# Kernel optimization log

Measured on AMD Instinct MI355X. Metric: run time of the kernel, lower is better.

## Reference

```python
import jax, jax.numpy as jnp
import numpy as np

N = 100000
E = 1600000
F_IN, HID, N_CLS = 128, 16, 32


def setup_inputs() -> dict:
    key = jax.random.key(0)
    ks = jax.random.split(key, 10)
    x = jax.random.normal(ks[0], (N, F_IN), dtype=jnp.float32)
    edge_index = jax.random.randint(ks[1], (2, E), 0, N, dtype=jnp.int64)
    edge_weight = jax.random.uniform(ks[2], (E,), dtype=jnp.float32)
    def glorot(k, shape):
        lim = np.sqrt(6.0 / (shape[0] + shape[1])).astype(np.float32)
        return jax.random.uniform(k, shape, dtype=jnp.float32, minval=-lim, maxval=lim)
    return {
        'x': x, 'edge_index': edge_index, 'edge_weight': edge_weight,
        'W1_0': glorot(ks[3], (F_IN, HID)), 'W1_1': glorot(ks[4], (F_IN, HID)),
        'b1': jnp.zeros((HID,), jnp.float32),
        'W2_0': glorot(ks[5], (HID, N_CLS)), 'W2_1': glorot(ks[6], (HID, N_CLS)),
        'b2': jnp.zeros((N_CLS,), jnp.float32),
    }


def _cheb_conv_k2(x, row, col, edge_weight, W0, W1, b):
    # PyG ChebConv, K=2, lambda_max=2.0:
    #   T0 = x; T1 = L_hat x = D^{-1/2} A D^{-1/2} x - x
    n = x.shape[0]
    deg = jax.ops.segment_sum(edge_weight, row, num_segments=n)  # [N]
    dinv = jnp.where(deg > 0, jax.lax.rsqrt(deg), 0.0)
    norm = dinv[row] * edge_weight * dinv[col]                   # [E]
    agg = jax.ops.segment_sum(norm[:, None] * x[col], row, num_segments=n)  # [N,F]
    tx1 = agg - x
    return x @ W0 + tx1 @ W1 + b


def reference(x, edge_index, edge_weight, W1_0, W1_1, b1, W2_0, W2_1, b2):
    row, col = edge_index[0], edge_index[1]
    h = jax.nn.relu(_cheb_conv_k2(x, row, col, edge_weight, W1_0, W1_1, b1))
    # dropout(p=0) and DFA layers are identity in forward
    out = _cheb_conv_k2(h, row, col, edge_weight, W2_0, W2_1, b2)
    return jax.nn.log_softmax(out, axis=1)
```

## Files before the change

kernel.cpp:

```cpp
#include <hip/hip_runtime.h>
#include <hip/hip_bf16.h>


#include <hip/hip_fp16.h>

constexpr int NN   = 100000;
constexpr int NE   = 1600000;
constexpr int FIN  = 128;
constexpr int HID  = 16;
constexpr int NCLS = 32;

constexpr int RB    = 256;
constexpr int NBKT  = (NN + RB - 1) / RB;
constexpr int EPB   = 4096;
constexpr int EPT   = EPB / 256;
constexpr int GP    = (NE + EPB - 1) / EPB;
constexpr int CAP   = 8192;
constexpr int NTILE = NN / 16;

typedef float f32x2 __attribute__((ext_vector_type(2)));
typedef float f32x4 __attribute__((ext_vector_type(4)));
typedef short bf16x8 __attribute__((ext_vector_type(8)));

#if defined(__has_builtin)
#if __has_builtin(__builtin_amdgcn_cvt_pk_f32_fp8)
#define HAVE_CVT_FP8 1
#endif
#endif

static __device__ __forceinline__ unsigned int f2e4m3(float f) {
    union { float f; unsigned int u; } v; v.f = f;
    unsigned int s = (v.u >> 24) & 0x80u;
    unsigned int au = v.u & 0x7fffffffu;
    if (au > 0x43E00000u) au = 0x43E00000u;
    au += 0x7ffffu + ((au >> 20) & 1u);
    int e4 = (int)(au >> 23) - 120;
    unsigned int m = (au >> 20) & 7u;
    unsigned int byte = (e4 <= 0) ? 0u : (((unsigned int)e4 << 3) | m);
    return s | byte;
}
static __device__ __forceinline__ void fp8x4_fma(unsigned int v, float w, float* acc) {
#ifdef HAVE_CVT_FP8
    f32x2 lo = __builtin_amdgcn_cvt_pk_f32_fp8((int)v, false);
    f32x2 hi = __builtin_amdgcn_cvt_pk_f32_fp8((int)v, true);
    acc[0] += w * lo.x; acc[1] += w * lo.y;
    acc[2] += w * hi.x; acc[3] += w * hi.y;
#else
#pragma unroll
    for (int i = 0; i < 4; i++) {
        unsigned int b = (v >> (8 * i)) & 0xffu;
        float f = __int_as_float((int)(((b & 0x80u) << 24) | ((b & 0x7fu) << 20))) * 0x1p120f;
        acc[i] += w * f;
    }
#endif
}
static __device__ __forceinline__ unsigned short f2bf(float f) {
    union { float f; unsigned int u; } v; v.f = f;
    unsigned int r = v.u + 0x7fffu + ((v.u >> 16) & 1u);
    return (unsigned short)(r >> 16);
}
static __device__ __forceinline__ unsigned int wpack(float wf) {
    unsigned int b = __float_as_uint(wf) + 0x8000u;
    return (b >> 16) & 0x7fffu;
}
static __device__ __forceinline__ float wdec(unsigned int u) {
    return __uint_as_float((u >> 17) << 16);
}

__global__ void k_zero_cur(int* __restrict__ bucketCursor) {
    int i = blockIdx.x * blockDim.x + threadIdx.x;
    if (i < NBKT) bucketCursor[i] = 0;
}

__global__ __launch_bounds__(256) void k_partition(
    const int* __restrict__ row, const int* __restrict__ col,
    const float* __restrict__ w, int* __restrict__ bucketCursor,
    int2* __restrict__ partS) {
    __shared__ int2 stage[EPB];
    __shared__ unsigned short sbkt[EPB];
    __shared__ int cnt[NBKT];
    __shared__ int lofs[NBKT];
    __shared__ int cursor[NBKT];
    __shared__ int gbase[NBKT];
    __shared__ int sa[512], sb[512];
    int tid = threadIdx.x;
    long ebase = (long)blockIdx.x * EPB;
    int rr[EPT]; int cc[EPT]; float wv[EPT];
#pragma unroll
    for (int i = 0; i < EPT; i++) {
        long e = ebase + i * 256 + tid;
        if (e < NE) { rr[i] = row[e]; cc[i] = col[e]; wv[i] = w[e]; }
        else rr[i] = -1;
    }
    for (int i = tid; i < NBKT; i += 256) cnt[i] = 0;
    __syncthreads();
#pragma unroll
    for (int i = 0; i < EPT; i++)
        if (rr[i] >= 0) atomicAdd(&cnt[rr[i] >> 8], 1);
    __syncthreads();
    for (int i = tid; i < 512; i += 256) sa[i] = (i < NBKT) ? cnt[i] : 0;
    __syncthreads();
    int* src = sa; int* dst = sb;
    for (int off = 1; off < 512; off <<= 1) {
        for (int i = tid; i < 512; i += 256)
            dst[i] = src[i] + ((i >= off) ? src[i - off] : 0);
        __syncthreads();
        int* t = src; src = dst; dst = t;
    }
    for (int i = tid; i < NBKT; i += 256) {
        int ex = src[i] - cnt[i];
        lofs[i] = ex;
        cursor[i] = ex;
        int go = (cnt[i] > 0) ? atomicAdd(&bucketCursor[i], cnt[i]) : 0;
        gbase[i] = i * CAP + go;
    }
    __syncthreads();
#pragma unroll
    for (int i = 0; i < EPT; i++) {
        if (rr[i] >= 0) {
            int b = rr[i] >> 8;
            int p = atomicAdd(&cursor[b], 1);
            int2 v;
            v.x = cc[i] | ((rr[i] & 255) << 17);
            v.y = __float_as_int(wv[i]);
            stage[p] = v;
            sbkt[p] = (unsigned short)b;
        }
    }
    __syncthreads();
    int total = (int)min((long)EPB, NE - ebase);
    for (int i = tid; i < total; i += 256) {
        int b = sbkt[i];
        partS[gbase[b] + (i - lofs[b])] = stage[i];
    }
}

__global__ void k_scan_buckets(const int* __restrict__ bucketCursor,
                               int* __restrict__ bucketStart) {
    int lane = threadIdx.x;
    int v[8], e[8];
    int s = 0;
#pragma unroll
    for (int t = 0; t < 8; t++) {
        int idx = lane * 8 + t;
        v[t] = (idx < NBKT) ? bucketCursor[idx] : 0;
        e[t] = s;
        s += v[t];
    }
    int sc = s;
    for (int off = 1; off < 64; off <<= 1) {
        int up = __shfl_up(sc, off, 64);
        if (lane >= off) sc += up;
    }
    int excl = sc - s;
#pragma unroll
    for (int t = 0; t < 8; t++) {
        int idx = lane * 8 + t;
        if (idx < NBKT) bucketStart[idx] = excl + e[t];
    }
}

__global__ __launch_bounds__(256) void k_bucket_sort(
    const int2* __restrict__ partS, const int* __restrict__ bucketCursor,
    const int* __restrict__ bucketStart,
    unsigned int* __restrict__ partC, int* __restrict__ rowptr,
    float* __restrict__ dinv) {
    __shared__ int2 stage[CAP];
    __shared__ int hist[RB];
    __shared__ int cursor[RB];
    __shared__ int wtot[4];
    int b = blockIdx.x;
    int tid = threadIdx.x;
    int start = bucketStart[b];
    int count = bucketCursor[b];
    const int2* src = partS + (long)b * CAP;
    hist[tid] = 0;
    __syncthreads();
    for (int i = tid; i < count; i += 256)
        atomicAdd(&hist[(src[i].x >> 17) & 255], 1);
    __syncthreads();
    int lane = tid & 63, wv = tid >> 6;
    int v = hist[tid];
    int sc = v;
#pragma unroll
    for (int off = 1; off < 64; off <<= 1) {
        int up = __shfl_up(sc, off, 64);
        if (lane >= off) sc += up;
    }
    if (lane == 63) wtot[wv] = sc;
    __syncthreads();
    int add = 0;
    for (int w2 = 0; w2 < wv; w2++) add += wtot[w2];
    int ex = sc + add - v;
    int node = b * RB + tid;
    if (node <= NN) rowptr[node] = start + ex;
    cursor[tid] = ex;
    __syncthreads();
    for (int i = tid; i < count; i += 256) {
        int2 p = src[i];
        int rl = (p.x >> 17) & 255;
        int pos = atomicAdd(&cursor[rl], 1);
        int2 c; c.x = p.x & 0x1FFFF; c.y = p.y;
        if (pos < CAP) stage[pos] = c;
    }
    __syncthreads();
    {
        int rend = cursor[tid];
        float d = 0.f;
        for (int i = ex; i < rend; i++) d += __int_as_float(stage[i].y);
        if (node < NN) dinv[node] = d > 0.f ? rsqrtf(d) : 0.f;
    }
    for (int i = tid; i < count; i += 256)
        if (i < CAP) {
            int2 p = stage[i];
            partC[start + i] = (unsigned int)p.x | (wpack(__int_as_float(p.y)) << 17);
        }
}

__global__ __launch_bounds__(256) void k_proj1(
    const float* __restrict__ x, const float* __restrict__ W0,
    const float* __restrict__ W1, const float* __restrict__ b1,
    const float* __restrict__ dinv,
    float* __restrict__ xa, unsigned char* __restrict__ xb8) {
    int wid = (int)(((long)blockIdx.x * 256 + threadIdx.x) >> 6);
    if (wid >= NTILE) return;
    int lane = threadIdx.x & 63;
    int col = lane & 15, quad = lane >> 4;

    bf16x8 bfrag[2][4];
#pragma unroll
    for (int mat = 0; mat < 2; mat++) {
        const float* W = mat ? W1 : W0;
#pragma unroll
        for (int kb = 0; kb < 4; kb++) {
            bf16x8 f;
#pragma unroll
            for (int j = 0; j < 8; j++)
                f[j] = (short)f2bf(W[(kb * 32 + quad * 8 + j) * HID + col]);
            bfrag[mat][kb] = f;
        }
    }

    const float* xrow = x + ((long)wid * 16 + col) * FIN + quad * 8;
    float4 xb[8];
#pragma unroll
    for (int kb = 0; kb < 4; kb++) {
        xb[2 * kb]     = *(const float4*)(xrow + kb * 32);
        xb[2 * kb + 1] = *(const float4*)(xrow + kb * 32 + 4);
    }
    f32x4 acc0 = {0.f, 0.f, 0.f, 0.f}, acc1 = {0.f, 0.f, 0.f, 0.f};
#pragma unroll
    for (int kb = 0; kb < 4; kb++) {
        float4 a0 = xb[2 * kb], a1 = xb[2 * kb + 1];
        bf16x8 af;
        af[0] = (short)f2bf(a0.x); af[1] = (short)f2bf(a0.y);
        af[2] = (short)f2bf(a0.z); af[3] = (short)f2bf(a0.w);
        af[4] = (short)f2bf(a1.x); af[5] = (short)f2bf(a1.y);
        af[6] = (short)f2bf(a1.z); af[7] = (short)f2bf(a1.w);
        acc0 = __builtin_amdgcn_mfma_f32_16x16x32_bf16(af, bfrag[0][kb], acc0, 0, 0, 0);
        acc1 = __builtin_amdgcn_mfma_f32_16x16x32_bf16(af, bfrag[1][kb], acc1, 0, 0, 0);
    }

    float b1v = b1[col];
#pragma unroll
    for (int r = 0; r < 4; r++) {
        long node = (long)wid * 16 + quad * 4 + r;
        float a0 = acc0[r], a1 = acc1[r];
        xa[node * HID + col] = a0 - a1 + b1v;
        float dn = dinv[node];
        xb8[node * HID + col] = (unsigned char)f2e4m3(dn * a1);
    }
}

__global__ __launch_bounds__(256) void k_gather1(
    const int* __restrict__ rowptr, const unsigned int* __restrict__ partC,
    const float* __restrict__ dinv, const unsigned char* __restrict__ xb8,
    float* __restrict__ agg1) {
    long t = (long)blockIdx.x * 256 + threadIdx.x;
    int n = (int)(t >> 6);
    if (n >= NN) return;
    int lane = threadIdx.x & 63;
    int d = lane & 3, p = lane >> 2;
    int s = rowptr[n], e = rowptr[n + 1];
    float acc[4] = {0.f, 0.f, 0.f, 0.f};
    for (int j = s + p; j < e; j += 16) {
        unsigned int u = partC[j];
        unsigned int v = *(const unsigned int*)(xb8 + (u & 0x1FFFF) * HID + d * 4);
        fp8x4_fma(v, wdec(u), acc);
    }
#pragma unroll
    for (int i = 0; i < 4; i++) {
        acc[i] += __shfl_xor(acc[i], 4);
        acc[i] += __shfl_xor(acc[i], 8);
        acc[i] += __shfl_xor(acc[i], 16);
        acc[i] += __shfl_xor(acc[i], 32);
    }
    if (p == 0) {
        float dn = dinv[n];
        float4 o; o.x = dn * acc[0]; o.y = dn * acc[1];
        o.z = dn * acc[2]; o.w = dn * acc[3];
        *(float4*)(agg1 + (long)n * HID + d * 4) = o;
    }
}

__global__ __launch_bounds__(256) void k_proj2(
    const float* __restrict__ xa, const float* __restrict__ agg1,
    const float* __restrict__ W0, const float* __restrict__ W1,
    const float* __restrict__ b2, const float* __restrict__ dinv,
    float* __restrict__ ha, unsigned char* __restrict__ hb8) {
    long n = (long)blockIdx.x * 256 + threadIdx.x;
    if (n >= NN) return;
    float h[HID];
    const float4* xap = (const float4*)(xa + n * HID);
    const float4* agp = (const float4*)(agg1 + n * HID);
#pragma unroll
    for (int q = 0; q < 4; q++) {
        float4 a = xap[q], g = agp[q];
        h[4*q+0] = fmaxf(a.x + g.x, 0.f);
        h[4*q+1] = fmaxf(a.y + g.y, 0.f);
        h[4*q+2] = fmaxf(a.z + g.z, 0.f);
        h[4*q+3] = fmaxf(a.w + g.w, 0.f);
    }
    float accA[NCLS], accB[NCLS];
#pragma unroll
    for (int o = 0; o < NCLS; o++) { accA[o] = 0.f; accB[o] = 0.f; }
#pragma unroll 2
    for (int k = 0; k < HID; k++) {
        float hk = h[k];
#pragma unroll
        for (int o = 0; o < NCLS; o++) accA[o] += hk * W0[k * NCLS + o];
#pragma unroll
        for (int o = 0; o < NCLS; o++) accB[o] += hk * W1[k * NCLS + o];
    }
    float4* hap = (float4*)(ha + n * NCLS);
#pragma unroll
    for (int q = 0; q < 8; q++) {
        float4 va;
        va.x = accA[4*q+0] - accB[4*q+0] + b2[4*q+0];
        va.y = accA[4*q+1] - accB[4*q+1] + b2[4*q+1];
        va.z = accA[4*q+2] - accB[4*q+2] + b2[4*q+2];
        va.w = accA[4*q+3] - accB[4*q+3] + b2[4*q+3];
        hap[q] = va;
    }
    float dn = dinv[n];
    unsigned int pk[8];
#pragma unroll
    for (int q = 0; q < 8; q++)
        pk[q] = f2e4m3(dn * accB[4*q+0]) | (f2e4m3(dn * accB[4*q+1]) << 8)
              | (f2e4m3(dn * accB[4*q+2]) << 16) | (f2e4m3(dn * accB[4*q+3]) << 24);
    uint4* hbp = (uint4*)(hb8 + n * NCLS);
    hbp[0] = make_uint4(pk[0], pk[1], pk[2], pk[3]);
    hbp[1] = make_uint4(pk[4], pk[5], pk[6], pk[7]);
}

__global__ __launch_bounds__(256) void k_gather2_lsm(
    const int* __restrict__ rowptr, const unsigned int* __restrict__ partC,
    const float* __restrict__ dinv, const float* __restrict__ ha,
    const unsigned char* __restrict__ hb8, float* __restrict__ out) {
    long t = (long)blockIdx.x * 256 + threadIdx.x;
    int n = (int)(t >> 6);
    if (n >= NN) return;
    int lane = threadIdx.x & 63;
    int d = lane & 7, p = lane >> 3;
    int s = rowptr[n], e = rowptr[n + 1];
    float acc[4] = {0.f, 0.f, 0.f, 0.f};
    int j = s + p;
    for (; j + 8 < e; j += 16) {
        unsigned int u0 = partC[j], u1 = partC[j + 8];
        unsigned int v0 = *(const unsigned int*)(hb8 + (u0 & 0x1FFFF) * NCLS + d * 4);
        unsigned int v1 = *(const unsigned int*)(hb8 + (u1 & 0x1FFFF) * NCLS + d * 4);
        fp8x4_fma(v0, wdec(u0), acc);
        fp8x4_fma(v1, wdec(u1), acc);
    }
    if (j < e) {
        unsigned int u0 = partC[j];
        unsigned int v0 = *(const unsigned int*)(hb8 + (u0 & 0x1FFFF) * NCLS + d * 4);
        fp8x4_fma(v0, wdec(u0), acc);
    }
#pragma unroll
    for (int i = 0; i < 4; i++) {
        acc[i] += __shfl_xor(acc[i], 8);
        acc[i] += __shfl_xor(acc[i], 16);
        acc[i] += __shfl_xor(acc[i], 32);
    }
    float dn = dinv[n];
    float4 hv = *(const float4*)(ha + (long)n * NCLS + d * 4);
    float v0 = dn * acc[0] + hv.x;
    float v1 = dn * acc[1] + hv.y;
    float v2 = dn * acc[2] + hv.z;
    float v3 = dn * acc[3] + hv.w;
    float m = fmaxf(fmaxf(v0, v1), fmaxf(v2, v3));
    m = fmaxf(m, __shfl_xor(m, 1));
    m = fmaxf(m, __shfl_xor(m, 2));
    m = fmaxf(m, __shfl_xor(m, 4));
    float sum = __expf(v0 - m) + __expf(v1 - m) + __expf(v2 - m) + __expf(v3 - m);
    sum += __shfl_xor(sum, 1);
    sum += __shfl_xor(sum, 2);
    sum += __shfl_xor(sum, 4);
    float ls = logf(sum);
    if (p == 0) {
        float4 o; o.x = v0 - m - ls; o.y = v1 - m - ls;
        o.z = v2 - m - ls; o.w = v3 - m - ls;
        *(float4*)(out + (long)n * NCLS + d * 4) = o;
    }
}

extern "C" void kernel_launch(void* const* d_in, const int* in_sizes, int n_in,
                              void* d_out, int out_size, void* d_ws, size_t ws_size,
                              hipStream_t stream) {
    const float* x    = (const float*)d_in[0];
    const int*   ei   = (const int*)d_in[1];
    const float* ew   = (const float*)d_in[2];
    const float* W1_0 = (const float*)d_in[3];
    const float* W1_1 = (const float*)d_in[4];
    const float* b1   = (const float*)d_in[5];
    const float* W2_0 = (const float*)d_in[6];
    const float* W2_1 = (const float*)d_in[7];
    const float* b2   = (const float*)d_in[8];
    float* out = (float*)d_out;

    const int* row = ei;
    const int* col = ei + NE;

    char* ws = (char*)d_ws;
    int2*  partS     = (int2*)ws;                 ws += sizeof(int2) * (long)NBKT * CAP;
    unsigned int* partC = (unsigned int*)ws;      ws += sizeof(int) * NE;
    int*   bucketCursor = (int*)ws;               ws += sizeof(int) * NBKT;
    int*   bucketStart  = (int*)ws;               ws += sizeof(int) * NBKT;
    int*   rowptr    = (int*)ws;                  ws += sizeof(int) * (NN + 4);
    float* dinv      = (float*)ws;                ws += sizeof(float) * NN;
    float* xa        = (float*)ws;                ws += sizeof(float) * NN * HID;
    float* agg1      = (float*)ws;                ws += sizeof(float) * NN * HID;
    float* ha        = (float*)ws;                ws += sizeof(float) * NN * NCLS;
    unsigned char* xb8 = (unsigned char*)ws;      ws += sizeof(char) * NN * HID;
    unsigned char* hb8 = (unsigned char*)ws;      ws += sizeof(char) * NN * NCLS;

    k_zero_cur<<<(NBKT + 255) / 256, 256, 0, stream>>>(bucketCursor);
    k_partition<<<GP, 256, 0, stream>>>(row, col, ew, bucketCursor, partS);
    k_scan_buckets<<<1, 64, 0, stream>>>(bucketCursor, bucketStart);
    k_bucket_sort<<<NBKT, 256, 0, stream>>>(partS, bucketCursor, bucketStart,
                                            partC, rowptr, dinv);
    k_proj1<<<(NTILE * 64 + 255) / 256, 256, 0, stream>>>(x, W1_0, W1_1, b1, dinv, xa, xb8);
    {
        long th = (long)NN * 64;
        k_gather1<<<(int)((th + 255) / 256), 256, 0, stream>>>(rowptr, partC, dinv, xb8, agg1);
    }
    k_proj2<<<(NN + 255) / 256, 256, 0, stream>>>(xa, agg1, W2_0, W2_1, b2, dinv, ha, hb8);
    {
        long th = (long)NN * 64;
        k_gather2_lsm<<<(int)((th + 255) / 256), 256, 0, stream>>>(rowptr, partC, dinv, ha, hb8, out);
    }
}
```

Baseline: 232.1 us.

## Fuse gather1 with proj2, fold bucket scan into sort, drop LDS staging

Three changes. The layer-2 projection is fused into the first gather kernel: each wavefront shuffles the 16 hidden values across lanes and computes 32 outputs per weight matrix, which removes the agg1 round trip through memory and one launch. The separate single-block bucket scan kernel is removed, and each sort block instead sums the counts of all earlier buckets itself, which is redundant O(NBKT) work per block. The sort now writes partC directly from the per-row atomic positions and accumulates degree with LDS float atomics instead of staging in 64KB of shared memory. That should raise occupancy but makes the global writes scattered and the edge order within a row nondeterministic.

```diff
diff --git a/kernel.cpp b/kernel.cpp
--- a/kernel.cpp
+++ b/kernel.cpp
@@ -135,51 +135,32 @@
     }
 }
 
-__global__ void k_scan_buckets(const int* __restrict__ bucketCursor,
-                               int* __restrict__ bucketStart) {
-    int lane = threadIdx.x;
-    int v[8], e[8];
-    int s = 0;
-#pragma unroll
-    for (int t = 0; t < 8; t++) {
-        int idx = lane * 8 + t;
-        v[t] = (idx < NBKT) ? bucketCursor[idx] : 0;
-        e[t] = s;
-        s += v[t];
-    }
-    int sc = s;
-    for (int off = 1; off < 64; off <<= 1) {
-        int up = __shfl_up(sc, off, 64);
-        if (lane >= off) sc += up;
-    }
-    int excl = sc - s;
-#pragma unroll
-    for (int t = 0; t < 8; t++) {
-        int idx = lane * 8 + t;
-        if (idx < NBKT) bucketStart[idx] = excl + e[t];
-    }
-}
-
 __global__ __launch_bounds__(256) void k_bucket_sort(
     const int2* __restrict__ partS, const int* __restrict__ bucketCursor,
-    const int* __restrict__ bucketStart,
     unsigned int* __restrict__ partC, int* __restrict__ rowptr,
     float* __restrict__ dinv) {
-    __shared__ int2 stage[CAP];
     __shared__ int hist[RB];
     __shared__ int cursor[RB];
+    __shared__ float dsum[RB];
     __shared__ int wtot[4];
+    __shared__ int red[4];
     int b = blockIdx.x;
     int tid = threadIdx.x;
-    int start = bucketStart[b];
+    int lane = tid & 63, wv = tid >> 6;
+    int partial = 0;
+    for (int i = tid; i < b; i += 256) partial += bucketCursor[i];
+#pragma unroll
+    for (int off = 1; off < 64; off <<= 1) partial += __shfl_xor(partial, off, 64);
+    if (lane == 0) red[wv] = partial;
+    hist[tid] = 0;
+    dsum[tid] = 0.f;
+    __syncthreads();
+    int start = red[0] + red[1] + red[2] + red[3];
     int count = bucketCursor[b];
     const int2* src = partS + (long)b * CAP;
-    hist[tid] = 0;
-    __syncthreads();
     for (int i = tid; i < count; i += 256)
-        atomicAdd(&hist[(src[i].x >> 17) & 255], 1);
-    __syncthreads();
-    int lane = tid & 63, wv = tid >> 6;
+        atomicAdd(&hist[((unsigned)src[i].x >> 17) & 255], 1);
+    __syncthreads();
     int v = hist[tid];
     int sc = v;
 #pragma unroll
@@ -198,23 +179,17 @@
     __syncthreads();
     for (int i = tid; i < count; i += 256) {
         int2 p = src[i];
-        int rl = (p.x >> 17) & 255;
+        int rl = ((unsigned)p.x >> 17) & 255;
         int pos = atomicAdd(&cursor[rl], 1);
-        int2 c; c.x = p.x & 0x1FFFF; c.y = p.y;
-        if (pos < CAP) stage[pos] = c;
-    }
-    __syncthreads();
-    {
-        int rend = cursor[tid];
-        float d = 0.f;
-        for (int i = ex; i < rend; i++) d += __int_as_float(stage[i].y);
-        if (node < NN) dinv[node] = d > 0.f ? rsqrtf(d) : 0.f;
-    }
-    for (int i = tid; i < count; i += 256)
-        if (i < CAP) {
-            int2 p = stage[i];
-            partC[start + i] = (unsigned int)p.x | (wpack(__int_as_float(p.y)) << 17);
-        }
+        float wf = __int_as_float(p.y);
+        partC[start + pos] = ((unsigned)p.x & 0x1FFFFu) | (wpack(wf) << 17);
+        atomicAdd(&dsum[rl], wf);
+    }
+    __syncthreads();
+    if (node < NN) {
+        float dsv = dsum[tid];
+        dinv[node] = dsv > 0.f ? rsqrtf(dsv) : 0.f;
+    }
 }
 
 __global__ __launch_bounds__(256) void k_proj1(
@@ -272,10 +247,12 @@
     }
 }
 
-__global__ __launch_bounds__(256) void k_gather1(
+__global__ __launch_bounds__(256) void k_gather1_proj2(
     const int* __restrict__ rowptr, const unsigned int* __restrict__ partC,
     const float* __restrict__ dinv, const unsigned char* __restrict__ xb8,
-    float* __restrict__ agg1) {
+    const float* __restrict__ xa, const float* __restrict__ W0,
+    const float* __restrict__ W1, const float* __restrict__ b2,
+    float* __restrict__ ha, unsigned char* __restrict__ hb8) {
     long t = (long)blockIdx.x * 256 + threadIdx.x;
     int n = (int)(t >> 6);
     if (n >= NN) return;
@@ -295,62 +272,37 @@
         acc[i] += __shfl_xor(acc[i], 16);
         acc[i] += __shfl_xor(acc[i], 32);
     }
-    if (p == 0) {
-        float dn = dinv[n];
-        float4 o; o.x = dn * acc[0]; o.y = dn * acc[1];
-        o.z = dn * acc[2]; o.w = dn * acc[3];
-        *(float4*)(agg1 + (long)n * HID + d * 4) = o;
-    }
-}
-
-__global__ __launch_bounds__(256) void k_proj2(
-    const float* __restrict__ xa, const float* __restrict__ agg1,
-    const float* __restrict__ W0, const float* __restrict__ W1,
-    const float* __restrict__ b2, const float* __restrict__ dinv,
-    float* __restrict__ ha, unsigned char* __restrict__ hb8) {
-    long n = (long)blockIdx.x * 256 + threadIdx.x;
-    if (n >= NN) return;
-    float h[HID];
-    const float4* xap = (const float4*)(xa + n * HID);
-    const float4* agp = (const float4*)(agg1 + n * HID);
-#pragma unroll
-    for (int q = 0; q < 4; q++) {
-        float4 a = xap[q], g = agp[q];
-        h[4*q+0] = fmaxf(a.x + g.x, 0.f);
-        h[4*q+1] = fmaxf(a.y + g.y, 0.f);
-        h[4*q+2] = fmaxf(a.z + g.z, 0.f);
-        h[4*q+3] = fmaxf(a.w + g.w, 0.f);
-    }
-    float accA[NCLS], accB[NCLS];
-#pragma unroll
-    for (int o = 0; o < NCLS; o++) { accA[o] = 0.f; accB[o] = 0.f; }
-#pragma unroll 2
-    for (int k = 0; k < HID; k++) {
-        float hk = h[k];
-#pragma unroll
-        for (int o = 0; o < NCLS; o++) accA[o] += hk * W0[k * NCLS + o];
-#pragma unroll
-        for (int o = 0; o < NCLS; o++) accB[o] += hk * W1[k * NCLS + o];
-    }
-    float4* hap = (float4*)(ha + n * NCLS);
-#pragma unroll
-    for (int q = 0; q < 8; q++) {
-        float4 va;
-        va.x = accA[4*q+0] - accB[4*q+0] + b2[4*q+0];
-        va.y = accA[4*q+1] - accB[4*q+1] + b2[4*q+1];
-        va.z = accA[4*q+2] - accB[4*q+2] + b2[4*q+2];
-        va.w = accA[4*q+3] - accB[4*q+3] + b2[4*q+3];
-        hap[q] = va;
-    }
     float dn = dinv[n];
-    unsigned int pk[8];
-#pragma unroll
-    for (int q = 0; q < 8; q++)
-        pk[q] = f2e4m3(dn * accB[4*q+0]) | (f2e4m3(dn * accB[4*q+1]) << 8)
-              | (f2e4m3(dn * accB[4*q+2]) << 16) | (f2e4m3(dn * accB[4*q+3]) << 24);
-    uint4* hbp = (uint4*)(hb8 + n * NCLS);
-    hbp[0] = make_uint4(pk[0], pk[1], pk[2], pk[3]);
-    hbp[1] = make_uint4(pk[4], pk[5], pk[6], pk[7]);
+    float4 xav = *(const float4*)(xa + (long)n * HID + d * 4);
+    float hq0 = fmaxf(xav.x + dn * acc[0], 0.f);
+    float hq1 = fmaxf(xav.y + dn * acc[1], 0.f);
+    float hq2 = fmaxf(xav.z + dn * acc[2], 0.f);
+    float hq3 = fmaxf(xav.w + dn * acc[3], 0.f);
+    float h[16];
+#pragma unroll
+    for (int a = 0; a < 4; a++) {
+        h[4 * a + 0] = __shfl(hq0, a, 64);
+        h[4 * a + 1] = __shfl(hq1, a, 64);
+        h[4 * a + 2] = __shfl(hq2, a, 64);
+        h[4 * a + 3] = __shfl(hq3, a, 64);
+    }
+    int m = lane >> 5, o = lane & 31;
+    const float* Wm = m ? W1 : W0;
+    float acc2 = 0.f;
+#pragma unroll
+    for (int k = 0; k < HID; k++) acc2 += h[k] * Wm[k * NCLS + o];
+    float other = __shfl_xor(acc2, 32);
+    if (m == 0) {
+        ha[(long)n * NCLS + o] = acc2 - other + b2[o];
+    } else {
+        unsigned int b0 = f2e4m3(dn * acc2);
+        unsigned int b1v = __shfl_down(b0, 1);
+        unsigned int b2v = __shfl_down(b0, 2);
+        unsigned int b3v = __shfl_down(b0, 3);
+        if ((o & 3) == 0)
+            *(unsigned int*)(hb8 + (long)n * NCLS + o) =
+                b0 | (b1v << 8) | (b2v << 16) | (b3v << 24);
+    }
 }
 
 __global__ __launch_bounds__(256) void k_gather2_lsm(
@@ -426,26 +378,22 @@
     int2*  partS     = (int2*)ws;                 ws += sizeof(int2) * (long)NBKT * CAP;
     unsigned int* partC = (unsigned int*)ws;      ws += sizeof(int) * NE;
     int*   bucketCursor = (int*)ws;               ws += sizeof(int) * NBKT;
-    int*   bucketStart  = (int*)ws;               ws += sizeof(int) * NBKT;
     int*   rowptr    = (int*)ws;                  ws += sizeof(int) * (NN + 4);
     float* dinv      = (float*)ws;                ws += sizeof(float) * NN;
     float* xa        = (float*)ws;                ws += sizeof(float) * NN * HID;
-    float* agg1      = (float*)ws;                ws += sizeof(float) * NN * HID;
     float* ha        = (float*)ws;                ws += sizeof(float) * NN * NCLS;
     unsigned char* xb8 = (unsigned char*)ws;      ws += sizeof(char) * NN * HID;
     unsigned char* hb8 = (unsigned char*)ws;      ws += sizeof(char) * NN * NCLS;
 
     k_zero_cur<<<(NBKT + 255) / 256, 256, 0, stream>>>(bucketCursor);
     k_partition<<<GP, 256, 0, stream>>>(row, col, ew, bucketCursor, partS);
-    k_scan_buckets<<<1, 64, 0, stream>>>(bucketCursor, bucketStart);
-    k_bucket_sort<<<NBKT, 256, 0, stream>>>(partS, bucketCursor, bucketStart,
-                                            partC, rowptr, dinv);
+    k_bucket_sort<<<NBKT, 256, 0, stream>>>(partS, bucketCursor, partC, rowptr, dinv);
     k_proj1<<<(NTILE * 64 + 255) / 256, 256, 0, stream>>>(x, W1_0, W1_1, b1, dinv, xa, xb8);
     {
         long th = (long)NN * 64;
-        k_gather1<<<(int)((th + 255) / 256), 256, 0, stream>>>(rowptr, partC, dinv, xb8, agg1);
-    }
-    k_proj2<<<(NN + 255) / 256, 256, 0, stream>>>(xa, agg1, W2_0, W2_1, b2, dinv, ha, hb8);
+        k_gather1_proj2<<<(int)((th + 255) / 256), 256, 0, stream>>>(
+            rowptr, partC, dinv, xb8, xa, W2_0, W2_1, b2, ha, hb8);
+    }
     {
         long th = (long)NN * 64;
         k_gather2_lsm<<<(int)((th + 255) / 256), 256, 0, stream>>>(rowptr, partC, dinv, ha, hb8, out);
```

After: 231.4 us. Within noise of the previous version (-0.3%).
